# Kernel tuning notes

Hardware: AMD Instinct MI355X
Metric: run time of the kernel (lower is better)

Reference implementation:

```python
import math
import jax, jax.numpy as jnp
import numpy as np

B, N, DIM = 2, 4096, 768
H, DK, DV = 8, 64, 64


def setup_inputs() -> dict:
    key = jax.random.key(0)
    ks = jax.random.split(key, 6)
    s = 0.02
    return {
        "x": jax.random.normal(ks[0], (B, N, DIM), dtype=jnp.float32),
        "Wq": jax.random.normal(ks[1], (DIM, H * DK), dtype=jnp.float32) * s,
        "Wk": jax.random.normal(ks[2], (DIM, H * DK), dtype=jnp.float32) * s,
        "Wv": jax.random.normal(ks[3], (DIM, H * DV), dtype=jnp.float32) * s,
        "Wo": jax.random.normal(ks[4], (H * DV, DIM), dtype=jnp.float32) * s,
        "bo": jax.random.normal(ks[5], (DIM,), dtype=jnp.float32) * s,
    }


def reference(x, Wq, Wk, Wv, Wo, bo):
    b, n, _ = x.shape
    # project and split heads: [B, H, N, d]
    q = (x @ Wq).reshape(b, n, H, DK).transpose(0, 2, 1, 3)
    k = (x @ Wk).reshape(b, n, H, DK).transpose(0, 2, 1, 3)
    v = (x @ Wv).reshape(b, n, H, DV).transpose(0, 2, 1, 3)
    scale = 1.0 / math.sqrt(DK)
    scores = jnp.einsum("bhnd,bhmd->bhnm", q, k) * scale  # [B,H,N,N]
    attn = jax.nn.softmax(scores, axis=-1)
    out = jnp.einsum("bhnm,bhmd->bhnd", attn, v)  # [B,H,N,DV]
    out = out.transpose(0, 2, 1, 3).reshape(b, n, H * DV)
    return out @ Wo + bo
```

## Files before the change

kernel.cpp:

```cpp
#include <hip/hip_runtime.h>
#include <hip/hip_bf16.h>

#define B_   2
#define N_   4096
#define DIM_ 768
#define H_   8
#define MROWS_ 8192

typedef __bf16 bf16x8 __attribute__((ext_vector_type(8)));
typedef __bf16 bf16x4 __attribute__((ext_vector_type(4)));
typedef float  f32x4  __attribute__((ext_vector_type(4)));

static __device__ __forceinline__ f32x4 mfma16(bf16x8 a, bf16x8 b, f32x4 c) {
    return __builtin_amdgcn_mfma_f32_16x16x32_bf16(a, b, c, 0, 0, 0);
}

#define GLDS16(g, l) \
    __builtin_amdgcn_global_load_lds((const __attribute__((address_space(1))) void*)(g), \
                                     (__attribute__((address_space(3))) void*)(l), 16, 0, 0)

__global__ void cvt_x_kernel(const float* __restrict__ x, __bf16* __restrict__ xb, int n4) {
    int i = blockIdx.x * blockDim.x + threadIdx.x;
    if (i >= n4) return;
    float4 f = reinterpret_cast<const float4*>(x)[i];
    bf16x4 o;
    o[0] = (__bf16)f.x; o[1] = (__bf16)f.y; o[2] = (__bf16)f.z; o[3] = (__bf16)f.w;
    reinterpret_cast<bf16x4*>(xb)[i] = o;
}

__global__ __launch_bounds__(256) void transpose_w_kernel(const float* __restrict__ Wq,
                                                          const float* __restrict__ Wk,
                                                          const float* __restrict__ Wv,
                                                          const float* __restrict__ Wo,
                                                          __bf16* __restrict__ wt,
                                                          __bf16* __restrict__ wot) {
    __shared__ float tile[64][65];
    const int bix = blockIdx.x;
    const float* src;
    int src_ld, rbase, cbase, dst_ld, drow, dcol;
    __bf16* dst;
    if (bix < 288) {
        int m = bix / 96, t = bix - m * 96;
        int tr = t >> 3, tc = t & 7;
        src = (m == 0) ? Wq : ((m == 1) ? Wk : Wv);
        src_ld = 512; rbase = tr * 64; cbase = tc * 64;
        dst = wt; dst_ld = 768; drow = m * 512 + tc * 64; dcol = tr * 64;
    } else {
        int t = bix - 288;
        int tr = t / 12, tc = t - tr * 12;
        src = Wo; src_ld = 768; rbase = tr * 64; cbase = tc * 64;
        dst = wot; dst_ld = 512; drow = tc * 64; dcol = tr * 64;
    }
#pragma unroll
    for (int kk = 0; kk < 4; ++kk) {
        int idx = threadIdx.x + kk * 256;
        int r = idx >> 4, c = (idx & 15) << 2;
        float4 f = *reinterpret_cast<const float4*>(&src[(size_t)(rbase + r) * src_ld + cbase + c]);
        tile[r][c] = f.x; tile[r][c + 1] = f.y; tile[r][c + 2] = f.z; tile[r][c + 3] = f.w;
    }
    __syncthreads();
#pragma unroll
    for (int kk = 0; kk < 4; ++kk) {
        int idx = threadIdx.x + kk * 256;
        int r = idx >> 4, c = (idx & 15) << 2;
        bf16x4 ov;
        ov[0] = (__bf16)tile[c][r];     ov[1] = (__bf16)tile[c + 1][r];
        ov[2] = (__bf16)tile[c + 2][r]; ov[3] = (__bf16)tile[c + 3][r];
        *reinterpret_cast<bf16x4*>(&dst[(size_t)(drow + r) * dst_ld + dcol + c]) = ov;
    }
}

template<int KSTEPS>
__device__ __forceinline__ void gemm_tile_main(const __bf16* __restrict__ A, const int lda,
                                               const int arow0,
                                               const __bf16* __restrict__ Bt, const int ldb,
                                               const int bcol0,
                                               __bf16* __restrict__ abuf,
                                               __bf16* __restrict__ bbuf,
                                               f32x4 (&acc)[4][4]) {
    const int lane = threadIdx.x & 63, wave = threadIdx.x >> 6;
    const int lr = lane & 15, lg = lane >> 4;
    const int wr = wave >> 1, wc = wave & 1;

    const int cid0 = wave * 128 + lane;
    const int cid1 = cid0 + 64;
    const __bf16* sA0 = A  + (size_t)(arow0 + (cid0 >> 2)) * lda + (cid0 & 3) * 8;
    const __bf16* sA1 = A  + (size_t)(arow0 + (cid1 >> 2)) * lda + (cid1 & 3) * 8;
    const __bf16* sB0 = Bt + (size_t)(bcol0 + (cid0 >> 2)) * ldb + (cid0 & 3) * 8;
    const __bf16* sB1 = Bt + (size_t)(bcol0 + (cid1 >> 2)) * ldb + (cid1 & 3) * 8;

    auto stage = [&](int buf, int ks) {
        __bf16* da = abuf + buf * 4096 + wave * 1024;
        __bf16* db = bbuf + buf * 4096 + wave * 1024;
        GLDS16(sA0 + ks * 32, da);
        GLDS16(sA1 + ks * 32, da + 512);
        GLDS16(sB0 + ks * 32, db);
        GLDS16(sB1 + ks * 32, db + 512);
    };

    stage(0, 0);
    asm volatile("s_waitcnt vmcnt(0)" ::: "memory");
    __syncthreads();

    const int ar_off = (wr * 64 + lr) * 32 + lg * 8;
    const int br_off = (wc * 64 + lr) * 32 + lg * 8;

    int buf = 0;
    for (int ks = 0; ks < KSTEPS; ++ks) {
        if (ks + 1 < KSTEPS) stage(buf ^ 1, ks + 1);
        const __bf16* ab = abuf + buf * 4096 + ar_off;
        const __bf16* bb = bbuf + buf * 4096 + br_off;
        bf16x8 af[4], bfr[4];
#pragma unroll
        for (int m = 0; m < 4; ++m) af[m] = *reinterpret_cast<const bf16x8*>(ab + m * 512);
#pragma unroll
        for (int n = 0; n < 4; ++n) bfr[n] = *reinterpret_cast<const bf16x8*>(bb + n * 512);
#pragma unroll
        for (int m = 0; m < 4; ++m)
#pragma unroll
            for (int n = 0; n < 4; ++n)
                acc[m][n] = mfma16(af[m], bfr[n], acc[m][n]);
        asm volatile("s_waitcnt vmcnt(0)" ::: "memory");
        __syncthreads();
        buf ^= 1;
    }
}

__global__ __launch_bounds__(256) void qkv_gemm_kernel(const __bf16* __restrict__ xb,
                                                       const __bf16* __restrict__ wt,
                                                       __bf16* __restrict__ q,
                                                       __bf16* __restrict__ k,
                                                       __bf16* __restrict__ vt) {
    __shared__ __align__(16) __bf16 abuf[2 * 4096];
    __shared__ __align__(16) __bf16 bbuf[2 * 4096];

    const int bid = blockIdx.x;
    const int vb = (bid & 7) * 96 + (bid >> 3);
    const int by = vb % 12, bx = vb / 12;

    f32x4 acc[4][4] = {};
    gemm_tile_main<24>(xb, 768, bx * 128, wt, 768, by * 128, abuf, bbuf, acc);

    const int lane = threadIdx.x & 63, wave = threadIdx.x >> 6;
    const int lr = lane & 15, lg = lane >> 4;
    const int wr = wave >> 1, wc = wave & 1;
    const int bi = (bx * 128) >> 12;
    const int nbase = (bx * 128) & 4095;

    const float QSCALE = 0.125f * 1.44269504089f;

#pragma unroll
    for (int n = 0; n < 4; ++n) {
        const int col0 = by * 128 + wc * 64 + n * 16;
        const int mtx = col0 >> 9;
        const int h   = (col0 >> 6) & 7;
        const int d0  = (col0 & 63) + lr;
        const size_t hb = (size_t)(bi * 8 + h);
#pragma unroll
        for (int m = 0; m < 4; ++m) {
            const int nn = nbase + wr * 64 + m * 16 + lg * 4;
            if (mtx == 0) {
#pragma unroll
                for (int r = 0; r < 4; ++r)
                    q[(hb * 4096 + nn + r) * 64 + d0] = (__bf16)(acc[m][n][r] * QSCALE);
            } else if (mtx == 1) {
#pragma unroll
                for (int r = 0; r < 4; ++r)
                    k[(hb * 4096 + nn + r) * 64 + d0] = (__bf16)acc[m][n][r];
            } else {
                bf16x4 ov;
#pragma unroll
                for (int r = 0; r < 4; ++r) ov[r] = (__bf16)acc[m][n][r];
                *reinterpret_cast<bf16x4*>(&vt[(hb * 64 + d0) * 4096 + nn]) = ov;
            }
        }
    }
}

__global__ __launch_bounds__(256) void attn_kernel(const __bf16* __restrict__ q,
                                                   const __bf16* __restrict__ k,
                                                   const __bf16* __restrict__ vt,
                                                   __bf16* __restrict__ o) {
    const int lane = threadIdx.x & 63, wave = threadIdx.x >> 6;
    const int lr = lane & 15, lg = lane >> 4;

    const int bid  = blockIdx.x;
    const int vbid = (bid & 7) * 64 + (bid >> 3);
    const int qtile = vbid & 31;
    const int bh    = vbid >> 5;
    const int qbase = qtile * 128 + wave * 32;

    const __bf16* Qh = q  + (size_t)bh * N_ * 64;
    const __bf16* Kh = k  + (size_t)bh * N_ * 64;
    const __bf16* Vh = vt + (size_t)bh * 64 * N_;

    __shared__ __align__(16) __bf16 kbuf[2][64][64];
    __shared__ __align__(16) __bf16 vbuf[2][64][64];

    const int l8 = lane >> 3, l7 = lane & 7;
    const int swz8 = (l7 ^ l8) * 8;

    int ksrc[4];
#pragma unroll
    for (int c = 0; c < 4; ++c) {
        int i = (wave & 1) * 32 + c * 8 + l8;
        int sig = ((i >> 4) & 1) * 32 + ((i >> 2) & 3) * 8 + ((i >> 5) & 1) * 4 + (i & 3);
        ksrc[c] = sig * 64 + swz8;
    }

    auto stageK = [&](int buf, int jt) {
        if (wave < 2) {
            const __bf16* srcb = Kh + (size_t)jt * 64 * 64;
            __bf16* dst = &kbuf[buf][wave * 32][0];
#pragma unroll
            for (int c = 0; c < 4; ++c)
                GLDS16(srcb + ksrc[c], dst + c * 512);
        }
    };
    auto stageV = [&](int buf, int jt) {
        if (wave >= 2) {
            const int w2 = wave - 2;
            const __bf16* src = Vh + (size_t)(w2 * 32 + l8) * 4096 + jt * 64 + swz8;
            __bf16* dst = &vbuf[buf][w2 * 32][0];
#pragma unroll
            for (int c = 0; c < 4; ++c)
                GLDS16(src + (size_t)c * 8 * 4096, dst + c * 512);
        }
    };

    bf16x8 qf[2][2];
#pragma unroll
    for (int frag = 0; frag < 2; ++frag)
#pragma unroll
        for (int kc = 0; kc < 2; ++kc)
            qf[frag][kc] = *reinterpret_cast<const bf16x8*>(
                Qh + (size_t)(qbase + frag * 16 + lr) * 64 + kc * 32 + lg * 8);

    f32x4 acc[2][4] = {};
    f32x4 accl[2] = {};
    bf16x8 vones;
#pragma unroll
    for (int t = 0; t < 8; ++t) vones[t] = (__bf16)1.0f;

    auto QK = [&](f32x4 (&s)[2][4], const __bf16* kb_) {
        const char* kb = (const char*)kb_;
        __builtin_amdgcn_s_setprio(1);
#pragma unroll
        for (int kc = 0; kc < 2; ++kc) {
#pragma unroll
            for (int cb = 0; cb < 4; ++cb) {
                const int row = cb * 16 + lr;
                bf16x8 bk = *reinterpret_cast<const bf16x8*>(
                    kb + row * 128 + (((kc * 4 + lg) ^ (lr & 7)) << 4));
                if (kc == 0) { s[0][cb] = mfma16(bk, qf[0][0], {}); s[1][cb] = mfma16(bk, qf[1][0], {}); }
                else         { s[0][cb] = mfma16(bk, qf[0][1], s[0][cb]); s[1][cb] = mfma16(bk, qf[1][1], s[1][cb]); }
            }
        }
        __builtin_amdgcn_s_setprio(0);
    };
    auto EXP = [&](f32x4 (&s)[2][4], bf16x8 (&pk)[2][2]) {
#pragma unroll
        for (int frag = 0; frag < 2; ++frag)
#pragma unroll
            for (int kc = 0; kc < 2; ++kc) {
#pragma unroll
                for (int t = 0; t < 8; ++t)
                    pk[frag][kc][t] = (__bf16)__builtin_amdgcn_exp2f(s[frag][kc + 2 * (t >> 2)][t & 3]);
                accl[frag] = mfma16(pk[frag][kc], vones, accl[frag]);
            }
    };
    auto PV = [&](bf16x8 (&pk)[2][2], const __bf16* vb_) {
        const char* vb = (const char*)vb_;
        __builtin_amdgcn_s_setprio(1);
#pragma unroll
        for (int kc = 0; kc < 2; ++kc) {
#pragma unroll
            for (int cbv = 0; cbv < 4; ++cbv) {
                const int row = cbv * 16 + lr;
                bf16x8 bv = *reinterpret_cast<const bf16x8*>(
                    vb + row * 128 + (((kc * 4 + lg) ^ (lr & 7)) << 4));
                acc[0][cbv] = mfma16(pk[0][kc], bv, acc[0][cbv]);
                acc[1][cbv] = mfma16(pk[1][kc], bv, acc[1][cbv]);
            }
        }
        __builtin_amdgcn_s_setprio(0);
    };

    f32x4 sA[2][4], sB[2][4];
    bf16x8 pkA[2][2], pkB[2][2];

    stageK(0, 0);
    asm volatile("s_waitcnt vmcnt(0)" ::: "memory");
    __syncthreads();

    stageK(1, 1);
    stageV(0, 0);
    QK(sA, &kbuf[0][0][0]);
    asm volatile("s_waitcnt vmcnt(0)" ::: "memory");
    __syncthreads();

    for (int t = 0; t < 31; ++t) {
        const int jt = 2 * t + 1;
        stageK(0, jt + 1);
        stageV(1, jt);
        EXP(sA, pkA);
        QK(sB, &kbuf[1][0][0]);
        PV(pkA, &vbuf[0][0][0]);
        asm volatile("s_waitcnt vmcnt(0)" ::: "memory");
        __syncthreads();
        stageK(1, jt + 2);
        stageV(0, jt + 1);
        EXP(sB, pkB);
        QK(sA, &kbuf[0][0][0]);
        PV(pkB, &vbuf[1][0][0]);
        asm volatile("s_waitcnt vmcnt(0)" ::: "memory");
        __syncthreads();
    }

    stageV(1, 63);
    EXP(sA, pkA);
    QK(sB, &kbuf[1][0][0]);
    PV(pkA, &vbuf[0][0][0]);
    asm volatile("s_waitcnt vmcnt(0)" ::: "memory");
    __syncthreads();

    EXP(sB, pkB);
    PV(pkB, &vbuf[1][0][0]);

    const int b = bh >> 3, h = bh & 7;
#pragma unroll
    for (int frag = 0; frag < 2; ++frag) {
#pragma unroll
        for (int r = 0; r < 4; ++r) {
            float inv = 1.f / accl[frag][r];
            int row = b * N_ + qbase + frag * 16 + lg * 4 + r;
#pragma unroll
            for (int cbv = 0; cbv < 4; ++cbv)
                o[(size_t)row * 512 + h * 64 + cbv * 16 + lr] =
                    (__bf16)(acc[frag][cbv][r] * inv);
        }
    }
}

__global__ __launch_bounds__(256) void out_gemm_kernel(const __bf16* __restrict__ ob,
                                                       const __bf16* __restrict__ wot,
                                                       const float* __restrict__ bo,
                                                       float* __restrict__ out) {
    __shared__ __align__(16) __bf16 abuf[2 * 4096];
    __shared__ __align__(16) __bf16 bbuf[2 * 4096];

    const int bid = blockIdx.x;
    const int vb = (bid & 7) * 48 + (bid >> 3);
    const int by = vb % 6, bx = vb / 6;

    f32x4 acc[4][4] = {};
    gemm_tile_main<16>(ob, 512, bx * 128, wot, 512, by * 128, abuf, bbuf, acc);

    const int lane = threadIdx.x & 63, wave = threadIdx.x >> 6;
    const int lr = lane & 15, lg = lane >> 4;
    const int wr = wave >> 1, wc = wave & 1;

#pragma unroll
    for (int n = 0; n < 4; ++n) {
        const int col = by * 128 + wc * 64 + n * 16 + lr;
        const float bias = bo[col];
#pragma unroll
        for (int m = 0; m < 4; ++m) {
            const int row0 = bx * 128 + wr * 64 + m * 16 + lg * 4;
#pragma unroll
            for (int r = 0; r < 4; ++r)
                out[(size_t)(row0 + r) * 768 + col] = acc[m][n][r] + bias;
        }
    }
}

extern "C" void kernel_launch(void* const* d_in, const int* in_sizes, int n_in,
                              void* d_out, int out_size, void* d_ws, size_t ws_size,
                              hipStream_t stream) {
    const float* x  = (const float*)d_in[0];
    const float* Wq = (const float*)d_in[1];
    const float* Wk = (const float*)d_in[2];
    const float* Wv = (const float*)d_in[3];
    const float* Wo = (const float*)d_in[4];
    const float* bo = (const float*)d_in[5];
    float* out = (float*)d_out;

    char* ws = (char*)d_ws;
    __bf16* xb  = (__bf16*)(ws);
    __bf16* wt  = (__bf16*)(ws + 12582912);
    __bf16* wot = (__bf16*)(ws + 12582912 + 2359296);
    char*   p0  = ws + 12582912 + 2359296 + 786432;
    __bf16* qw  = (__bf16*)(p0);
    __bf16* kw  = (__bf16*)(p0 + 8388608);
    __bf16* vtw = (__bf16*)(p0 + 2 * (size_t)8388608);
    __bf16* obf = (__bf16*)(p0 + 3 * (size_t)8388608);

    cvt_x_kernel<<<6144, 256, 0, stream>>>(x, xb, MROWS_ * DIM_ / 4);
    transpose_w_kernel<<<384, 256, 0, stream>>>(Wq, Wk, Wv, Wo, wt, wot);
    qkv_gemm_kernel<<<768, 256, 0, stream>>>(xb, wt, qw, kw, vtw);
    attn_kernel<<<512, 256, 0, stream>>>(qw, kw, vtw, obf);
    out_gemm_kernel<<<384, 256, 0, stream>>>(obf, wot, bo, out);
}
```

Before: 125.0 us.

## Stage two KV tiles per barrier with 4-slot LDS ping-pong to halve syncs

Doubles the K and V shared-memory buffers so that each loop iteration prefetches two 64-row tiles and computes two tiles between barriers. This halves the number of vmcnt waits and workgroup barriers. It also replaces __syncthreads with a raw s_barrier, using read and write offsets that flip between the halves. LDS use doubles to 64KB, which may reduce occupancy, and the prologue and epilogue tile indexing is reworked to match.

```diff
diff --git a/kernel.cpp b/kernel.cpp
--- a/kernel.cpp
+++ b/kernel.cpp
@@ -194,8 +194,10 @@
     const __bf16* Kh = k  + (size_t)bh * N_ * 64;
     const __bf16* Vh = vt + (size_t)bh * 64 * N_;
 
-    __shared__ __align__(16) __bf16 kbuf[2][64][64];
-    __shared__ __align__(16) __bf16 vbuf[2][64][64];
+    __shared__ __align__(16) __bf16 kbuf[2][2][64][64];
+    __shared__ __align__(16) __bf16 vbuf[2][2][64][64];
+    __bf16* kb0 = &kbuf[0][0][0][0];
+    __bf16* vb0 = &vbuf[0][0][0][0];
 
     const int l8 = lane >> 3, l7 = lane & 7;
     const int swz8 = (l7 ^ l8) * 8;
@@ -208,20 +210,20 @@
         ksrc[c] = sig * 64 + swz8;
     }
 
-    auto stageK = [&](int buf, int jt) {
+    auto stageK1 = [&](__bf16* dstbase, int jt) {
         if (wave < 2) {
-            const __bf16* srcb = Kh + (size_t)jt * 64 * 64;
-            __bf16* dst = &kbuf[buf][wave * 32][0];
+            const __bf16* srcb = Kh + (size_t)jt * 4096;
+            __bf16* dst = dstbase + (wave & 1) * 2048;
 #pragma unroll
             for (int c = 0; c < 4; ++c)
                 GLDS16(srcb + ksrc[c], dst + c * 512);
         }
     };
-    auto stageV = [&](int buf, int jt) {
+    auto stageV1 = [&](__bf16* dstbase, int jt) {
         if (wave >= 2) {
             const int w2 = wave - 2;
             const __bf16* src = Vh + (size_t)(w2 * 32 + l8) * 4096 + jt * 64 + swz8;
-            __bf16* dst = &vbuf[buf][w2 * 32][0];
+            __bf16* dst = dstbase + w2 * 2048;
 #pragma unroll
             for (int c = 0; c < 4; ++c)
                 GLDS16(src + (size_t)c * 8 * 4096, dst + c * 512);
@@ -289,43 +291,51 @@
     f32x4 sA[2][4], sB[2][4];
     bf16x8 pkA[2][2], pkB[2][2];
 
-    stageK(0, 0);
+    int rdo = 8192, wro = 0;
+
+    stageK1(kb0 + 8192, 0);
+    stageK1(kb0 + 8192 + 4096, 1);
+    stageV1(vb0 + 8192 + 4096, 0);
     asm volatile("s_waitcnt vmcnt(0)" ::: "memory");
-    __syncthreads();
-
-    stageK(1, 1);
-    stageV(0, 0);
-    QK(sA, &kbuf[0][0][0]);
+    __builtin_amdgcn_s_barrier();
+
+    stageK1(kb0 + wro, 2);          stageK1(kb0 + wro + 4096, 3);
+    stageV1(vb0 + wro, 1);          stageV1(vb0 + wro + 4096, 2);
+    QK(sB, kb0 + rdo);
+    EXP(sB, pkB);
+    QK(sA, kb0 + rdo + 4096);
+    PV(pkB, vb0 + rdo + 4096);
     asm volatile("s_waitcnt vmcnt(0)" ::: "memory");
-    __syncthreads();
-
-    for (int t = 0; t < 31; ++t) {
-        const int jt = 2 * t + 1;
-        stageK(0, jt + 1);
-        stageV(1, jt);
+    __builtin_amdgcn_s_barrier();
+    rdo ^= 8192; wro ^= 8192;
+
+    for (int P = 1; P <= 30; ++P) {
+        const int a = 2 * P;
+        stageK1(kb0 + wro, a + 2);      stageK1(kb0 + wro + 4096, a + 3);
+        stageV1(vb0 + wro, a + 1);      stageV1(vb0 + wro + 4096, a + 2);
         EXP(sA, pkA);
-        QK(sB, &kbuf[1][0][0]);
-        PV(pkA, &vbuf[0][0][0]);
+        QK(sB, kb0 + rdo);
+        PV(pkA, vb0 + rdo);
+        EXP(sB, pkB);
+        QK(sA, kb0 + rdo + 4096);
+        PV(pkB, vb0 + rdo + 4096);
         asm volatile("s_waitcnt vmcnt(0)" ::: "memory");
-        __syncthreads();
-        stageK(1, jt + 2);
-        stageV(0, jt + 1);
-        EXP(sB, pkB);
-        QK(sA, &kbuf[0][0][0]);
-        PV(pkB, &vbuf[1][0][0]);
-        asm volatile("s_waitcnt vmcnt(0)" ::: "memory");
-        __syncthreads();
-    }
-
-    stageV(1, 63);
+        __builtin_amdgcn_s_barrier();
+        rdo ^= 8192; wro ^= 8192;
+    }
+
+    stageV1(vb0 + wro, 63);
     EXP(sA, pkA);
-    QK(sB, &kbuf[1][0][0]);
-    PV(pkA, &vbuf[0][0][0]);
+    QK(sB, kb0 + rdo);
+    PV(pkA, vb0 + rdo);
+    EXP(sB, pkB);
+    QK(sA, kb0 + rdo + 4096);
+    PV(pkB, vb0 + rdo + 4096);
     asm volatile("s_waitcnt vmcnt(0)" ::: "memory");
-    __syncthreads();
-
-    EXP(sB, pkB);
-    PV(pkB, &vbuf[1][0][0]);
+    __builtin_amdgcn_s_barrier();
+
+    EXP(sA, pkA);
+    PV(pkA, vb0 + wro);
 
     const int b = bh >> 3, h = bh & 7;
 #pragma unroll
```

New measurement: 128.8 us. 3.0% more time.

## Split attention over two key halves and add a combine kernel

Applied to the files above, without the earlier changes.

Each (batch, head, query-tile) is now handled by two blocks, each covering half of the key/value sequence. This doubles the attention grid so more blocks run per CU, and raises the occupancy hint in launch bounds. Each split writes unnormalised bf16 partial outputs and row sums into reused workspace. A new combine kernel adds the two partials and divides by the summed normaliser. The trade-off is an extra kernel launch plus additional global traffic for the partials. The combine simply adds the two halves, which is only exact if the exponentials use a shared fixed offset rather than a per-split running max.

```diff
diff --git a/kernel.cpp b/kernel.cpp
--- a/kernel.cpp
+++ b/kernel.cpp
@@ -177,22 +177,27 @@
     }
 }
 
-__global__ __launch_bounds__(256) void attn_kernel(const __bf16* __restrict__ q,
-                                                   const __bf16* __restrict__ k,
-                                                   const __bf16* __restrict__ vt,
-                                                   __bf16* __restrict__ o) {
+__global__ __launch_bounds__(256, 4) void attn_kernel(const __bf16* __restrict__ q,
+                                                      const __bf16* __restrict__ k,
+                                                      const __bf16* __restrict__ vt,
+                                                      __bf16* __restrict__ part0,
+                                                      __bf16* __restrict__ part1,
+                                                      float* __restrict__ lsums) {
     const int lane = threadIdx.x & 63, wave = threadIdx.x >> 6;
     const int lr = lane & 15, lg = lane >> 4;
 
     const int bid  = blockIdx.x;
-    const int vbid = (bid & 7) * 64 + (bid >> 3);
-    const int qtile = vbid & 31;
-    const int bh    = vbid >> 5;
+    const int vbid = (bid & 7) * 128 + (bid >> 3);
+    const int bh    = vbid >> 6;
+    const int qs    = vbid & 63;
+    const int qtile = qs >> 1;
+    const int split = qs & 1;
     const int qbase = qtile * 128 + wave * 32;
+    const int kt0   = split * 32;
 
     const __bf16* Qh = q  + (size_t)bh * N_ * 64;
-    const __bf16* Kh = k  + (size_t)bh * N_ * 64;
-    const __bf16* Vh = vt + (size_t)bh * 64 * N_;
+    const __bf16* Kh = k  + (size_t)bh * N_ * 64 + (size_t)kt0 * 4096;
+    const __bf16* Vh = vt + (size_t)bh * 64 * N_ + kt0 * 64;
 
     __shared__ __align__(16) __bf16 kbuf[2][64][64];
     __shared__ __align__(16) __bf16 vbuf[2][64][64];
@@ -210,8 +215,8 @@
 
     auto stageK = [&](int buf, int jt) {
         if (wave < 2) {
-            const __bf16* srcb = Kh + (size_t)jt * 64 * 64;
-            __bf16* dst = &kbuf[buf][wave * 32][0];
+            const __bf16* srcb = Kh + (size_t)jt * 4096;
+            __bf16* dst = &kbuf[buf][(wave & 1) * 32][0];
 #pragma unroll
             for (int c = 0; c < 4; ++c)
                 GLDS16(srcb + ksrc[c], dst + c * 512);
@@ -299,7 +304,7 @@
     asm volatile("s_waitcnt vmcnt(0)" ::: "memory");
     __syncthreads();
 
-    for (int t = 0; t < 31; ++t) {
+    for (int t = 0; t < 15; ++t) {
         const int jt = 2 * t + 1;
         stageK(0, jt + 1);
         stageV(1, jt);
@@ -317,7 +322,7 @@
         __syncthreads();
     }
 
-    stageV(1, 63);
+    stageV(1, 31);
     EXP(sA, pkA);
     QK(sB, &kbuf[1][0][0]);
     PV(pkA, &vbuf[0][0][0]);
@@ -327,19 +332,45 @@
     EXP(sB, pkB);
     PV(pkB, &vbuf[1][0][0]);
 
+    __bf16* po = split ? part1 : part0;
+    float*  ls = lsums + (size_t)split * 65536;
     const int b = bh >> 3, h = bh & 7;
 #pragma unroll
     for (int frag = 0; frag < 2; ++frag) {
 #pragma unroll
         for (int r = 0; r < 4; ++r) {
-            float inv = 1.f / accl[frag][r];
-            int row = b * N_ + qbase + frag * 16 + lg * 4 + r;
+            const int qrow = qbase + frag * 16 + lg * 4 + r;
+            const int row = b * N_ + qrow;
 #pragma unroll
             for (int cbv = 0; cbv < 4; ++cbv)
-                o[(size_t)row * 512 + h * 64 + cbv * 16 + lr] =
-                    (__bf16)(acc[frag][cbv][r] * inv);
-        }
-    }
+                po[(size_t)row * 512 + h * 64 + cbv * 16 + lr] = (__bf16)acc[frag][cbv][r];
+            if (lr == 0)
+                ls[bh * 4096 + qrow] = accl[frag][r];
+        }
+    }
+}
+
+__global__ __launch_bounds__(256) void combine_kernel(__bf16* __restrict__ p0,
+                                                      const __bf16* __restrict__ p1,
+                                                      const float* __restrict__ lsums) {
+    const int g = blockIdx.x * 256 + threadIdx.x;
+    const int row = g >> 6;
+    const int col8 = g & 63;
+    const int h = col8 >> 3;
+    const int b = row >> 12;
+    const int qr = row & 4095;
+    const int bhq = (b * 8 + h) * 4096 + qr;
+    const float l = lsums[bhq] + lsums[65536 + bhq];
+    const float inv = 1.f / l;
+
+    const size_t off = (size_t)row * 512 + col8 * 8;
+    bf16x8 a0 = *reinterpret_cast<const bf16x8*>(p0 + off);
+    bf16x8 a1 = *reinterpret_cast<const bf16x8*>(p1 + off);
+    bf16x8 ov;
+#pragma unroll
+    for (int t = 0; t < 8; ++t)
+        ov[t] = (__bf16)(((float)a0[t] + (float)a1[t]) * inv);
+    *reinterpret_cast<bf16x8*>(p0 + off) = ov;
 }
 
 __global__ __launch_bounds__(256) void out_gemm_kernel(const __bf16* __restrict__ ob,
@@ -394,10 +425,13 @@
     __bf16* kw  = (__bf16*)(p0 + 8388608);
     __bf16* vtw = (__bf16*)(p0 + 2 * (size_t)8388608);
     __bf16* obf = (__bf16*)(p0 + 3 * (size_t)8388608);
+    __bf16* part1 = (__bf16*)(ws);
+    float*  lsums = (float*)(ws + 8388608);
 
     cvt_x_kernel<<<6144, 256, 0, stream>>>(x, xb, MROWS_ * DIM_ / 4);
     transpose_w_kernel<<<384, 256, 0, stream>>>(Wq, Wk, Wv, Wo, wt, wot);
-    qkv_gemm_kernel<<<768, 256, 0, stream>>>(xb, wt, qw, kw, vtw);
-    attn_kernel<<<512, 256, 0, stream>>>(qw, kw, vtw, obf);
+    qkv_gemm_kernel<<<dim3(768), 256, 0, stream>>>(xb, wt, qw, kw, vtw);
+    attn_kernel<<<1024, 256, 0, stream>>>(qw, kw, vtw, obf, part1, lsums);
+    combine_kernel<<<2048, 256, 0, stream>>>(obf, part1, lsums);
     out_gemm_kernel<<<384, 256, 0, stream>>>(obf, wot, bo, out);
 }
```

After: 215.3 us. +72.2%, slower.

## Split KV columns across wave pairs with 64-row query tiles and LDS reduction

Applied to the files above, without the earlier changes.

Each wave now handles 64 query rows but only half of every 64-key tile: waves are paired by query group, and each wave of a pair takes alternating 16-column key blocks. Every K/V fragment read from LDS now feeds four query fragments instead of two, which cuts LDS read traffic per MFMA. At the end, the partial outputs and row sums of the two waves in a pair are merged through shared memory. The two-stage software pipeline is reduced to a single-stage loop, the odd wave's partials are rounded to bf16 before the merge, and register pressure rises with 4x4 accumulators.

```diff
diff --git a/kernel.cpp b/kernel.cpp
--- a/kernel.cpp
+++ b/kernel.cpp
@@ -183,19 +183,21 @@
                                                    __bf16* __restrict__ o) {
     const int lane = threadIdx.x & 63, wave = threadIdx.x >> 6;
     const int lr = lane & 15, lg = lane >> 4;
+    const int qg = wave >> 1, kh = wave & 1;
 
     const int bid  = blockIdx.x;
     const int vbid = (bid & 7) * 64 + (bid >> 3);
     const int qtile = vbid & 31;
     const int bh    = vbid >> 5;
-    const int qbase = qtile * 128 + wave * 32;
+    const int qbase = qtile * 128 + qg * 64;
 
     const __bf16* Qh = q  + (size_t)bh * N_ * 64;
     const __bf16* Kh = k  + (size_t)bh * N_ * 64;
     const __bf16* Vh = vt + (size_t)bh * 64 * N_;
 
-    __shared__ __align__(16) __bf16 kbuf[2][64][64];
-    __shared__ __align__(16) __bf16 vbuf[2][64][64];
+    __shared__ __align__(16) char smem[32768];
+    __bf16* kb0 = (__bf16*)smem;
+    __bf16* vb0 = (__bf16*)(smem + 16384);
 
     const int l8 = lane >> 3, l7 = lane & 7;
     const int swz8 = (l7 ^ l8) * 8;
@@ -210,8 +212,8 @@
 
     auto stageK = [&](int buf, int jt) {
         if (wave < 2) {
-            const __bf16* srcb = Kh + (size_t)jt * 64 * 64;
-            __bf16* dst = &kbuf[buf][wave * 32][0];
+            const __bf16* srcb = Kh + (size_t)jt * 4096;
+            __bf16* dst = kb0 + buf * 4096 + (wave & 1) * 2048;
 #pragma unroll
             for (int c = 0; c < 4; ++c)
                 GLDS16(srcb + ksrc[c], dst + c * 512);
@@ -221,73 +223,72 @@
         if (wave >= 2) {
             const int w2 = wave - 2;
             const __bf16* src = Vh + (size_t)(w2 * 32 + l8) * 4096 + jt * 64 + swz8;
-            __bf16* dst = &vbuf[buf][w2 * 32][0];
+            __bf16* dst = vb0 + buf * 4096 + w2 * 2048;
 #pragma unroll
             for (int c = 0; c < 4; ++c)
                 GLDS16(src + (size_t)c * 8 * 4096, dst + c * 512);
         }
     };
 
-    bf16x8 qf[2][2];
-#pragma unroll
-    for (int frag = 0; frag < 2; ++frag)
+    bf16x8 qf[4][2];
+#pragma unroll
+    for (int f = 0; f < 4; ++f)
 #pragma unroll
         for (int kc = 0; kc < 2; ++kc)
-            qf[frag][kc] = *reinterpret_cast<const bf16x8*>(
-                Qh + (size_t)(qbase + frag * 16 + lr) * 64 + kc * 32 + lg * 8);
-
-    f32x4 acc[2][4] = {};
-    f32x4 accl[2] = {};
+            qf[f][kc] = *reinterpret_cast<const bf16x8*>(
+                Qh + (size_t)(qbase + f * 16 + lr) * 64 + kc * 32 + lg * 8);
+
+    f32x4 acc[4][4] = {};
+    f32x4 accl[4] = {};
     bf16x8 vones;
 #pragma unroll
     for (int t = 0; t < 8; ++t) vones[t] = (__bf16)1.0f;
 
-    auto QK = [&](f32x4 (&s)[2][4], const __bf16* kb_) {
+    f32x4 s[4][2];
+    bf16x8 pk[4];
+
+    auto QK = [&](const __bf16* kb_) {
         const char* kb = (const char*)kb_;
         __builtin_amdgcn_s_setprio(1);
 #pragma unroll
         for (int kc = 0; kc < 2; ++kc) {
 #pragma unroll
-            for (int cb = 0; cb < 4; ++cb) {
-                const int row = cb * 16 + lr;
+            for (int c2 = 0; c2 < 2; ++c2) {
+                const int row = (kh + 2 * c2) * 16 + lr;
                 bf16x8 bk = *reinterpret_cast<const bf16x8*>(
                     kb + row * 128 + (((kc * 4 + lg) ^ (lr & 7)) << 4));
-                if (kc == 0) { s[0][cb] = mfma16(bk, qf[0][0], {}); s[1][cb] = mfma16(bk, qf[1][0], {}); }
-                else         { s[0][cb] = mfma16(bk, qf[0][1], s[0][cb]); s[1][cb] = mfma16(bk, qf[1][1], s[1][cb]); }
+#pragma unroll
+                for (int f = 0; f < 4; ++f) {
+                    if (kc == 0) s[f][c2] = mfma16(bk, qf[f][0], {});
+                    else         s[f][c2] = mfma16(bk, qf[f][1], s[f][c2]);
+                }
             }
         }
         __builtin_amdgcn_s_setprio(0);
     };
-    auto EXP = [&](f32x4 (&s)[2][4], bf16x8 (&pk)[2][2]) {
-#pragma unroll
-        for (int frag = 0; frag < 2; ++frag)
-#pragma unroll
-            for (int kc = 0; kc < 2; ++kc) {
-#pragma unroll
-                for (int t = 0; t < 8; ++t)
-                    pk[frag][kc][t] = (__bf16)__builtin_amdgcn_exp2f(s[frag][kc + 2 * (t >> 2)][t & 3]);
-                accl[frag] = mfma16(pk[frag][kc], vones, accl[frag]);
-            }
-    };
-    auto PV = [&](bf16x8 (&pk)[2][2], const __bf16* vb_) {
+    auto EXP = [&]() {
+#pragma unroll
+        for (int f = 0; f < 4; ++f) {
+#pragma unroll
+            for (int t = 0; t < 8; ++t)
+                pk[f][t] = (__bf16)__builtin_amdgcn_exp2f(s[f][t >> 2][t & 3]);
+            accl[f] = mfma16(pk[f], vones, accl[f]);
+        }
+    };
+    auto PV = [&](const __bf16* vb_) {
         const char* vb = (const char*)vb_;
         __builtin_amdgcn_s_setprio(1);
 #pragma unroll
-        for (int kc = 0; kc < 2; ++kc) {
-#pragma unroll
-            for (int cbv = 0; cbv < 4; ++cbv) {
-                const int row = cbv * 16 + lr;
-                bf16x8 bv = *reinterpret_cast<const bf16x8*>(
-                    vb + row * 128 + (((kc * 4 + lg) ^ (lr & 7)) << 4));
-                acc[0][cbv] = mfma16(pk[0][kc], bv, acc[0][cbv]);
-                acc[1][cbv] = mfma16(pk[1][kc], bv, acc[1][cbv]);
-            }
+        for (int cbv = 0; cbv < 4; ++cbv) {
+            const int row = cbv * 16 + lr;
+            bf16x8 bv = *reinterpret_cast<const bf16x8*>(
+                vb + row * 128 + (((kh * 4 + lg) ^ (lr & 7)) << 4));
+#pragma unroll
+            for (int f = 0; f < 4; ++f)
+                acc[f][cbv] = mfma16(pk[f], bv, acc[f][cbv]);
         }
         __builtin_amdgcn_s_setprio(0);
     };
-
-    f32x4 sA[2][4], sB[2][4];
-    bf16x8 pkA[2][2], pkB[2][2];
 
     stageK(0, 0);
     asm volatile("s_waitcnt vmcnt(0)" ::: "memory");
@@ -295,49 +296,65 @@
 
     stageK(1, 1);
     stageV(0, 0);
-    QK(sA, &kbuf[0][0][0]);
+    QK(kb0);
+    EXP();
     asm volatile("s_waitcnt vmcnt(0)" ::: "memory");
     __syncthreads();
 
-    for (int t = 0; t < 31; ++t) {
-        const int jt = 2 * t + 1;
-        stageK(0, jt + 1);
-        stageV(1, jt);
-        EXP(sA, pkA);
-        QK(sB, &kbuf[1][0][0]);
-        PV(pkA, &vbuf[0][0][0]);
+    for (int jt = 1; jt < 63; ++jt) {
+        stageK((jt + 1) & 1, jt + 1);
+        stageV(jt & 1, jt);
+        QK(kb0 + (jt & 1) * 4096);
+        PV(vb0 + ((jt - 1) & 1) * 4096);
+        EXP();
         asm volatile("s_waitcnt vmcnt(0)" ::: "memory");
         __syncthreads();
-        stageK(1, jt + 2);
-        stageV(0, jt + 1);
-        EXP(sB, pkB);
-        QK(sA, &kbuf[0][0][0]);
-        PV(pkB, &vbuf[1][0][0]);
-        asm volatile("s_waitcnt vmcnt(0)" ::: "memory");
-        __syncthreads();
     }
 
     stageV(1, 63);
-    EXP(sA, pkA);
-    QK(sB, &kbuf[1][0][0]);
-    PV(pkA, &vbuf[0][0][0]);
+    QK(kb0 + 4096);
+    PV(vb0);
+    EXP();
     asm volatile("s_waitcnt vmcnt(0)" ::: "memory");
     __syncthreads();
 
-    EXP(sB, pkB);
-    PV(pkB, &vbuf[1][0][0]);
-
-    const int b = bh >> 3, h = bh & 7;
-#pragma unroll
-    for (int frag = 0; frag < 2; ++frag) {
-#pragma unroll
-        for (int r = 0; r < 4; ++r) {
-            float inv = 1.f / accl[frag][r];
-            int row = b * N_ + qbase + frag * 16 + lg * 4 + r;
-#pragma unroll
-            for (int cbv = 0; cbv < 4; ++cbv)
-                o[(size_t)row * 512 + h * 64 + cbv * 16 + lr] =
-                    (__bf16)(acc[frag][cbv][r] * inv);
+    PV(vb0 + 4096);
+    __syncthreads();
+
+    char* ex = smem + qg * 13824;
+    if (kh == 1) {
+#pragma unroll
+        for (int f = 0; f < 4; ++f) {
+#pragma unroll
+            for (int cbv = 0; cbv < 4; ++cbv) {
+                bf16x4 p4;
+#pragma unroll
+                for (int r = 0; r < 4; ++r) p4[r] = (__bf16)acc[f][cbv][r];
+                *reinterpret_cast<bf16x4*>(ex + lane * 136 + (f * 4 + cbv) * 8) = p4;
+            }
+            *reinterpret_cast<f32x4*>(ex + 8704 + lane * 80 + f * 16) = accl[f];
+        }
+    }
+    __syncthreads();
+
+    if (kh == 0) {
+        const int b = bh >> 3, h = bh & 7;
+#pragma unroll
+        for (int f = 0; f < 4; ++f) {
+            f32x4 lp = *reinterpret_cast<const f32x4*>(ex + 8704 + lane * 80 + f * 16);
+            f32x4 inv;
+#pragma unroll
+            for (int r = 0; r < 4; ++r) inv[r] = 1.f / (accl[f][r] + lp[r]);
+#pragma unroll
+            for (int cbv = 0; cbv < 4; ++cbv) {
+                bf16x4 ap = *reinterpret_cast<const bf16x4*>(ex + lane * 136 + (f * 4 + cbv) * 8);
+#pragma unroll
+                for (int r = 0; r < 4; ++r) {
+                    const int row = b * N_ + qbase + f * 16 + lg * 4 + r;
+                    o[(size_t)row * 512 + h * 64 + cbv * 16 + lr] =
+                        (__bf16)((acc[f][cbv][r] + (float)ap[r]) * inv[r]);
+                }
+            }
         }
     }
 }
```

Result: slower. 127.8 us (+2.2%).
